# Kernel optimization log

Hardware: AMD Instinct MI355X
Metric: run time of the kernel (lower is better)

## Reference

```python
import jax, jax.numpy as jnp
import numpy as np

N_HEAD = 16
N_EMBD = 1024
TIME_EMBD = 64
EPS = 1e-5

def _ln(x, w, b):
    mu = jnp.mean(x, axis=-1, keepdims=True)
    var = jnp.mean(jnp.square(x - mu), axis=-1, keepdims=True)
    return (x - mu) * jax.lax.rsqrt(var + EPS) * w + b

def _gelu(x):
    return jax.nn.gelu(x, approximate=False)

def setup_inputs() -> dict:
    key = jax.random.key(0)
    ks = jax.random.split(key, 12)
    B, T, D, TE = 2, 2048, N_EMBD, TIME_EMBD
    C = D + TE  # 1088
    s = lambda fan_in: 1.0 / np.sqrt(fan_in)
    return {
        "z": jax.random.normal(ks[0], (B, T, D), jnp.float32),
        "t": jax.random.uniform(ks[1], (B,), jnp.float32),
        # time_mlp: Linear(1, TE) -> GELU -> Linear(TE, TE)
        "w_t1": jax.random.normal(ks[2], (1, TE), jnp.float32) * s(1),
        "b_t1": jnp.zeros((TE,), jnp.float32),
        "w_t2": jax.random.normal(ks[3], (TE, TE), jnp.float32) * s(TE),
        "b_t2": jnp.zeros((TE,), jnp.float32),
        # attention
        "ln_a_w": jnp.ones((C,), jnp.float32),
        "ln_a_b": jnp.zeros((C,), jnp.float32),
        "w_attn": jax.random.normal(ks[4], (C, 3 * D), jnp.float32) * s(C),
        "b_attn": jnp.zeros((3 * D,), jnp.float32),
        "w_proj": jax.random.normal(ks[5], (D, D), jnp.float32) * s(D),
        "b_proj": jnp.zeros((D,), jnp.float32),
        # mlp
        "ln_m_w": jnp.ones((C,), jnp.float32),
        "ln_m_b": jnp.zeros((C,), jnp.float32),
        "w_fc": jax.random.normal(ks[6], (C, 4 * D), jnp.float32) * s(C),
        "b_fc": jnp.zeros((4 * D,), jnp.float32),
        "w_fc2": jax.random.normal(ks[7], (4 * D, D), jnp.float32) * s(4 * D),
        "b_fc2": jnp.zeros((D,), jnp.float32),
    }

def reference(z, t, w_t1, b_t1, w_t2, b_t2, ln_a_w, ln_a_b, w_attn, b_attn,
              w_proj, b_proj, ln_m_w, ln_m_b, w_fc, b_fc, w_fc2, b_fc2):
    B, T, D = z.shape
    H, hd = N_HEAD, N_EMBD // N_HEAD
    # time embedding: [B, TE] broadcast over T
    t_emb = _gelu(t[:, None] @ w_t1 + b_t1) @ w_t2 + b_t2
    t_emb_bt = jnp.broadcast_to(t_emb[:, None, :], (B, T, TIME_EMBD))
    # --- attention with time-conditioned input ---
    zt = jnp.concatenate([z, t_emb_bt], axis=-1)            # [B,T,D+TE]
    x = _ln(zt, ln_a_w, ln_a_b)
    qkv = x @ w_attn + b_attn                               # [B,T,3D]
    q, k, v = jnp.split(qkv, 3, axis=-1)
    q = q.reshape(B, T, H, hd)
    k = k.reshape(B, T, H, hd)
    v = v.reshape(B, T, H, hd)
    att = jnp.einsum('bqhd,bkhd->bhqk', q, k) * (1.0 / np.sqrt(hd))
    mask = jnp.tril(jnp.ones((T, T), bool))
    att = jnp.where(mask, att, -jnp.inf)
    att = jax.nn.softmax(att, axis=-1)
    y = jnp.einsum('bhqk,bkhd->bqhd', att, v).reshape(B, T, D)
    h = y @ w_proj + b_proj                                 # [B,T,D]
    # --- mlp with time-conditioned input ---
    ht = jnp.concatenate([h, t_emb_bt], axis=-1)
    m = _ln(ht, ln_m_w, ln_m_b)
    dz = _gelu(m @ w_fc + b_fc) @ w_fc2 + b_fc2             # [B,T,D]
    return dz
```

## Files before the change

kernel.cpp:

```cpp
#include <hip/hip_runtime.h>
#include <stdint.h>
#include <math.h>

#define T_SEQ 2048
#define NHEAD 16
#define HD 64
#define DMODEL 1024
#define CDIM 1088
#define MROWS 4096

typedef uint16_t u16;
typedef __bf16 b8v __attribute__((ext_vector_type(8)));
typedef float f4v __attribute__((ext_vector_type(4)));

typedef __attribute__((address_space(3))) void lds_void;
typedef const __attribute__((address_space(1))) void glb_void;

#define GLL(g, l) __builtin_amdgcn_global_load_lds((glb_void*)(g), (lds_void*)(l), 16, 0, 0)

__device__ __forceinline__ float b2f(u16 u) {
  union { uint32_t i; float f; } c; c.i = ((uint32_t)u) << 16; return c.f;
}
__device__ __forceinline__ u16 f2b(float f) {
  union { float f; uint32_t i; } c; c.f = f;
  uint32_t x = c.i;
  return (u16)((x + 0x7fffu + ((x >> 16) & 1u)) >> 16);
}
__device__ __forceinline__ uint32_t cvt_pk_bf16(float lo, float hi) {
  uint32_t r;
  asm("v_cvt_pk_bf16_f32 %0, %1, %2" : "=v"(r) : "v"(lo), "v"(hi));
  return r;
}
__device__ __forceinline__ float exp2_hw(float x) {
  return __builtin_amdgcn_exp2f(x);
}
__device__ __forceinline__ float gelu_f(float x) {
  float ax = fabsf(x);
  float xs = ax * 0.70710678118654752f;
  float t = __frcp_rn(1.0f + 0.3275911f * xs);
  float poly = ((((1.061405429f * t - 1.453152027f) * t + 1.421413741f) * t
                 - 0.284496736f) * t + 0.254829592f) * t;
  float e = __expf(-xs * xs);
  float er = 1.0f - poly * e;
  er = copysignf(er, x);
  return 0.5f * x * (1.0f + er);
}

__global__ void time_mlp_kernel(const float* __restrict__ t, const float* __restrict__ w1,
                                const float* __restrict__ b1, const float* __restrict__ w2,
                                const float* __restrict__ b2, float* __restrict__ temb) {
  __shared__ float h1[2][64];
  int tid = threadIdx.x;
  int b = tid >> 6, i = tid & 63;
  float tv = t[b];
  h1[b][i] = gelu_f(tv * w1[i] + b1[i]);
  __syncthreads();
  float acc = b2[i];
  for (int k = 0; k < 64; ++k) acc += h1[b][k] * w2[k * 64 + i];
  temb[b * 64 + i] = acc;
}

__global__ __launch_bounds__(256) void transpose_kernel(const float* __restrict__ src,
                                                        u16* __restrict__ dst,
                                                        int R, int C) {
  __shared__ u16 tile[32][33];
  int tx = threadIdx.x & 31, ty = threadIdx.x >> 5;
  int c0 = blockIdx.x * 32, r0 = blockIdx.y * 32;
#pragma unroll
  for (int i = 0; i < 4; ++i) {
    int r = ty + i * 8;
    tile[r][tx] = f2b(src[(size_t)(r0 + r) * C + c0 + tx]);
  }
  __syncthreads();
#pragma unroll
  for (int i = 0; i < 4; ++i) {
    int c = ty + i * 8;
    dst[(size_t)(c0 + c) * R + r0 + tx] = tile[tx][c];
  }
}

__global__ __launch_bounds__(256) void add4_kernel(const float4* __restrict__ a,
                                                   const float4* __restrict__ b,
                                                   const float4* __restrict__ c,
                                                   const float4* __restrict__ d,
                                                   float4* __restrict__ o, int n4) {
  int i = blockIdx.x * 256 + threadIdx.x;
  if (i < n4) {
    float4 x = a[i], y = b[i], z = c[i], w = d[i];
    o[i] = float4{x.x + y.x + z.x + w.x, x.y + y.y + z.y + w.y,
                  x.z + y.z + z.z + w.z, x.w + y.w + z.w + w.w};
  }
}

__global__ __launch_bounds__(256) void ln_concat_kernel(const float* __restrict__ zf,
                                                        const float* __restrict__ zf2,
                                                        const float* __restrict__ temb,
                                                        const float* __restrict__ w,
                                                        const float* __restrict__ bvec,
                                                        u16* __restrict__ xout,
                                                        int mode) {
  __shared__ float red[4];
  int row = blockIdx.x;
  int b = row / T_SEQ;
  int tid = threadIdx.x;
  float v[5];
  float sum = 0.f;
#pragma unroll
  for (int i = 0; i < 5; ++i) {
    int c = tid + i * 256;
    float val = 0.f;
    if (c < CDIM) {
      if (c < DMODEL) {
        size_t idx = (size_t)row * DMODEL + c;
        if (mode == 1) val = zf[idx];
        else val = zf[idx] + zf2[idx];
      } else {
        val = temb[b * 64 + (c - DMODEL)];
      }
    }
    v[i] = val;
    sum += val;
  }
#pragma unroll
  for (int off = 32; off; off >>= 1) sum += __shfl_xor(sum, off, 64);
  int wv = tid >> 6, ln = tid & 63;
  if (ln == 0) red[wv] = sum;
  __syncthreads();
  float mean = (red[0] + red[1] + red[2] + red[3]) * (1.0f / CDIM);
  __syncthreads();
  float sq = 0.f;
#pragma unroll
  for (int i = 0; i < 5; ++i) {
    int c = tid + i * 256;
    if (c < CDIM) { float d = v[i] - mean; sq += d * d; }
  }
#pragma unroll
  for (int off = 32; off; off >>= 1) sq += __shfl_xor(sq, off, 64);
  if (ln == 0) red[wv] = sq;
  __syncthreads();
  float inv = rsqrtf((red[0] + red[1] + red[2] + red[3]) * (1.0f / CDIM) + 1e-5f);
#pragma unroll
  for (int i = 0; i < 5; ++i) {
    int c = tid + i * 256;
    if (c < CDIM)
      xout[(size_t)row * CDIM + c] = f2b((v[i] - mean) * inv * w[c] + bvec[c]);
  }
}

__global__ __launch_bounds__(512, 2) void gemm256_kernel(
    const u16* __restrict__ A, const u16* __restrict__ Bt,
    const float* __restrict__ bias,
    void* __restrict__ c0, void* __restrict__ c1,
    void* __restrict__ c2, void* __restrict__ c3,
    int M, int N, int K, int k_tiles, int do_gelu, int out_f32) {
  __shared__ u16 As[2][256 * 64];
  __shared__ u16 Bs[2][256 * 64];
  const int tid = threadIdx.x;
  const int wave = tid >> 6, lane = tid & 63;
  const int wr = wave >> 2, wc = wave & 3;
  const int lrow = lane & 15, quad = lane >> 4;

  int nxy = gridDim.x * gridDim.y;
  int bid = blockIdx.y * gridDim.x + blockIdx.x;
  int cpx = nxy >> 3;
  int swz = (bid & 7) * cpx + (bid >> 3);
  int bx = swz % gridDim.x, by = swz / gridDim.x;
  const int m0 = bx * 256, n0 = by * 256;
  const int kz = blockIdx.z;
  const int kb = kz * k_tiles * 64;
  const int NT = k_tiles;

  const int sr = tid >> 3;
  const int sc = ((tid & 7) ^ ((tid >> 3) & 7)) * 8;
  const u16* gA = A + (size_t)(m0 + sr) * K + kb + sc;
  const u16* gB = Bt + (size_t)(n0 + sr) * K + kb + sc;

  f4v acc[8][4] = {};
  b8v bq[2][4];

  auto STAGE_A = [&](int t, int h) {
    const u16* g = gA + (size_t)(h * 128) * K + t * 64;
    u16* l = (u16*)As[t & 1] + h * 8192 + (wave << 9);
    GLL(g, l);
    GLL(g + (size_t)64 * K, l + 4096);
  };
  auto STAGE_B = [&](int t, int h) {
    const u16* g = gB + (size_t)(h * 128) * K + t * 64;
    u16* l = (u16*)Bs[t & 1] + h * 8192 + (wave << 9);
    GLL(g, l);
    GLL(g + (size_t)64 * K, l + 4096);
  };

  STAGE_A(0, 0); STAGE_B(0, 0); STAGE_B(0, 1);
  STAGE_A(0, 1);
  if (NT > 1) { STAGE_A(1, 0); STAGE_B(1, 0); STAGE_B(1, 1); }
  if (NT > 1) asm volatile("s_waitcnt vmcnt(8)" ::: "memory");
  else        asm volatile("s_waitcnt vmcnt(2)" ::: "memory");
  __builtin_amdgcn_s_barrier();

  for (int t = 0; t < NT; ++t) {
    const char* abase = (const char*)As[t & 1];
    const char* bbase = (const char*)Bs[t & 1];
    const int asw = (lrow & 7) << 4;
    b8v af[4];

#pragma unroll
    for (int j = 0; j < 4; ++j)
      af[j] = *(const b8v*)(abase + (j * 32 + wr * 16 + lrow) * 128 + ((quad * 16) ^ asw));
#pragma unroll
    for (int n = 0; n < 4; ++n)
      bq[0][n] = *(const b8v*)(bbase + (wc * 64 + n * 16 + lrow) * 128 + ((quad * 16) ^ asw));
    if (t + 1 < NT) STAGE_A(t + 1, 1);
    __builtin_amdgcn_s_barrier();
    __builtin_amdgcn_s_setprio(1);
#pragma unroll
    for (int j = 0; j < 4; ++j)
#pragma unroll
      for (int n = 0; n < 4; ++n)
        acc[j][n] = __builtin_amdgcn_mfma_f32_16x16x32_bf16(bq[0][n], af[j], acc[j][n], 0, 0, 0);
    __builtin_amdgcn_s_setprio(0);
    __builtin_amdgcn_s_barrier();

#pragma unroll
    for (int j = 0; j < 4; ++j)
      af[j] = *(const b8v*)(abase + (j * 32 + wr * 16 + lrow) * 128 + ((64 + quad * 16) ^ asw));
#pragma unroll
    for (int n = 0; n < 4; ++n)
      bq[1][n] = *(const b8v*)(bbase + (wc * 64 + n * 16 + lrow) * 128 + ((64 + quad * 16) ^ asw));
    __builtin_amdgcn_s_barrier();
    __builtin_amdgcn_s_setprio(1);
#pragma unroll
    for (int j = 0; j < 4; ++j)
#pragma unroll
      for (int n = 0; n < 4; ++n)
        acc[j][n] = __builtin_amdgcn_mfma_f32_16x16x32_bf16(bq[1][n], af[j], acc[j][n], 0, 0, 0);
    __builtin_amdgcn_s_setprio(0);
    if (t + 1 < NT) asm volatile("s_waitcnt vmcnt(8)" ::: "memory");
    else            asm volatile("s_waitcnt vmcnt(0)" ::: "memory");
    __builtin_amdgcn_s_barrier();

#pragma unroll
    for (int j = 0; j < 4; ++j)
      af[j] = *(const b8v*)(abase + (128 + j * 32 + wr * 16 + lrow) * 128 + ((quad * 16) ^ asw));
    if (t + 2 < NT) { STAGE_B(t + 2, 0); STAGE_A(t + 2, 0); }
    __builtin_amdgcn_s_barrier();
    __builtin_amdgcn_s_setprio(1);
#pragma unroll
    for (int j = 0; j < 4; ++j)
#pragma unroll
      for (int n = 0; n < 4; ++n)
        acc[4 + j][n] = __builtin_amdgcn_mfma_f32_16x16x32_bf16(bq[0][n], af[j], acc[4 + j][n], 0, 0, 0);
    __builtin_amdgcn_s_setprio(0);
    __builtin_amdgcn_s_barrier();

#pragma unroll
    for (int j = 0; j < 4; ++j)
      af[j] = *(const b8v*)(abase + (128 + j * 32 + wr * 16 + lrow) * 128 + ((64 + quad * 16) ^ asw));
    if (t + 2 < NT) STAGE_B(t + 2, 1);
    __builtin_amdgcn_s_barrier();
    __builtin_amdgcn_s_setprio(1);
#pragma unroll
    for (int j = 0; j < 4; ++j)
#pragma unroll
      for (int n = 0; n < 4; ++n)
        acc[4 + j][n] = __builtin_amdgcn_mfma_f32_16x16x32_bf16(bq[1][n], af[j], acc[4 + j][n], 0, 0, 0);
    __builtin_amdgcn_s_setprio(0);
    if (t + 1 < NT) {
      if (t + 2 < NT) asm volatile("s_waitcnt vmcnt(8)" ::: "memory");
      else            asm volatile("s_waitcnt vmcnt(2)" ::: "memory");
    }
    __builtin_amdgcn_s_barrier();
  }

  void* Cout = (kz == 0) ? c0 : (kz == 1) ? c1 : (kz == 2) ? c2 : c3;
#pragma unroll
  for (int mh = 0; mh < 2; ++mh)
#pragma unroll
    for (int j = 0; j < 4; ++j) {
      int grow = m0 + mh * 128 + j * 32 + wr * 16 + lrow;
      size_t rb = (size_t)grow * N;
#pragma unroll
      for (int n = 0; n < 4; ++n) {
        int gcol = n0 + wc * 64 + n * 16 + quad * 4;
        float b0 = 0.f, b1 = 0.f, b2 = 0.f, b3 = 0.f;
        if (kz == 0) {
          float4 bv = *(const float4*)(bias + gcol);
          b0 = bv.x; b1 = bv.y; b2 = bv.z; b3 = bv.w;
        }
        f4v a = acc[mh * 4 + j][n];
        float v0 = a[0] + b0, v1 = a[1] + b1, v2 = a[2] + b2, v3 = a[3] + b3;
        if (do_gelu) {
          v0 = gelu_f(v0); v1 = gelu_f(v1); v2 = gelu_f(v2); v3 = gelu_f(v3);
        }
        if (out_f32) {
          *(float4*)((float*)Cout + rb + gcol) = float4{v0, v1, v2, v3};
        } else {
          ushort4 ov;
          ov.x = f2b(v0); ov.y = f2b(v1); ov.z = f2b(v2); ov.w = f2b(v3);
          *(ushort4*)((u16*)Cout + rb + gcol) = ov;
        }
      }
    }
}

__global__ __launch_bounds__(256) void gemm_splitk2_kernel(const u16* __restrict__ A,
                                                           const u16* __restrict__ Bt,
                                                           const float* __restrict__ bias,
                                                           float* __restrict__ C0,
                                                           float* __restrict__ C1,
                                                           int M, int N, int K, int Kc) {
  __shared__ u16 As[2][128 * 32];
  __shared__ u16 Bs[2][128 * 32];
  const int tid = threadIdx.x;
  const int wave = tid >> 6, lane = tid & 63;
  const int wr = wave >> 1, wc = wave & 1;
  const int m0 = blockIdx.x * 128;
  const int n0 = blockIdx.y * 128;
  const int kz = blockIdx.z;
  const int lrow = lane & 15, quad = lane >> 4;
  const int srow = lane >> 2, sseg = lane & 3;

  const u16* gA0 = A  + (size_t)(m0 + wave * 32 + srow) * K + kz * Kc + sseg * 8;
  const u16* gA1 = gA0 + (size_t)16 * K;
  const u16* gB0 = Bt + (size_t)(n0 + wave * 32 + srow) * K + kz * Kc + sseg * 8;
  const u16* gB1 = gB0 + (size_t)16 * K;
  const int la0 = (wave * 32) * 32, la1 = (wave * 32 + 16) * 32;

  f4v acc[4][4] = {};

  GLL(gA0, &As[0][la0]); GLL(gA1, &As[0][la1]);
  GLL(gB0, &Bs[0][la0]); GLL(gB1, &Bs[0][la1]);

  int cur = 0;
  for (int k0 = 0; k0 < Kc; k0 += 32) {
    __syncthreads();
    if (k0 + 32 < Kc) {
      int nxt = cur ^ 1;
      GLL(gA0 + k0 + 32, &As[nxt][la0]); GLL(gA1 + k0 + 32, &As[nxt][la1]);
      GLL(gB0 + k0 + 32, &Bs[nxt][la0]); GLL(gB1 + k0 + 32, &Bs[nxt][la1]);
    }
    b8v af[4], bfr[4];
#pragma unroll
    for (int mi = 0; mi < 4; ++mi)
      af[mi] = *(const b8v*)(&As[cur][(wr * 64 + mi * 16 + lrow) * 32 + quad * 8]);
#pragma unroll
    for (int ni = 0; ni < 4; ++ni)
      bfr[ni] = *(const b8v*)(&Bs[cur][(wc * 64 + ni * 16 + lrow) * 32 + quad * 8]);
#pragma unroll
    for (int mi = 0; mi < 4; ++mi)
#pragma unroll
      for (int ni = 0; ni < 4; ++ni)
        acc[mi][ni] = __builtin_amdgcn_mfma_f32_16x16x32_bf16(bfr[ni], af[mi], acc[mi][ni], 0, 0, 0);
    cur ^= 1;
  }

  float* C = kz ? C1 : C0;
#pragma unroll
  for (int mi = 0; mi < 4; ++mi) {
    int grow = m0 + wr * 64 + mi * 16 + lrow;
    size_t rb = (size_t)grow * N;
#pragma unroll
    for (int ni = 0; ni < 4; ++ni) {
      int gcol = n0 + wc * 64 + ni * 16 + quad * 4;
      float b0 = 0.f, b1 = 0.f, b2 = 0.f, b3 = 0.f;
      if (kz == 0) {
        float4 bv = *(const float4*)(bias + gcol);
        b0 = bv.x; b1 = bv.y; b2 = bv.z; b3 = bv.w;
      }
      *(float4*)(C + rb + gcol) = float4{acc[mi][ni][0] + b0, acc[mi][ni][1] + b1,
                                         acc[mi][ni][2] + b2, acc[mi][ni][3] + b3};
    }
  }
}

__global__ __launch_bounds__(512) void attn_mfma_kernel(const u16* __restrict__ qkv,
                                                        u16* __restrict__ y) {
  __shared__ u16 Ks[64 * 72];
  __shared__ u16 Vts[64 * 72];
  __shared__ u16 Ps[128 * 72];
  const int bh = blockIdx.x;
  const int b = bh >> 4, h = bh & 15;
  const int qt = 15 - (int)blockIdx.y;
  const int tid = threadIdx.x, w = tid >> 6, lane = tid & 63;
  const int lrow = lane & 15, quad = lane >> 4;
  const int q0 = qt * 128;
  const int qg = q0 + w * 16 + lrow;
  const int dchunk = 2 * qt + (w >> 2);

  b8v qf[2];
#pragma unroll
  for (int dc = 0; dc < 2; ++dc)
    qf[dc] = *(const b8v*)(qkv + (size_t)(b * T_SEQ + qg) * 3072 + h * 64 + dc * 32 + quad * 8);

  f4v oacc[4] = {};
  float mrun = -__builtin_inff(), lrun = 0.f;
  const float SC = 0.18033688011112042f;

  const int nch = 2 * qt + 2;
  for (int ct = 0; ct < nch; ++ct) {
    __syncthreads();
    {
      int r = tid >> 3, sg = tid & 7;
      const u16* src = qkv + (size_t)(b * T_SEQ + ct * 64 + r) * 3072 + h * 64 + 1024 + sg * 8;
      *(uint4*)(&Ks[r * 72 + sg * 8]) = *(const uint4*)(src);
    }
    {
      int pr = tid >> 4, half = (tid >> 3) & 1, dsg = tid & 7;
      int d0 = dsg * 8 + half * 4;
      const u16* v0 = qkv + (size_t)(b * T_SEQ + ct * 64 + 2 * pr) * 3072 + h * 64 + 2048 + d0;
      uint2 a = *(const uint2*)(v0);
      uint2 bb = *(const uint2*)(v0 + 3072);
      int keyp = (2 * pr) ^ (dsg * 8);
      u16* vb = &Vts[d0 * 72 + keyp];
      *(uint32_t*)(vb)           = __builtin_amdgcn_perm(bb.x, a.x, 0x05040100u);
      *(uint32_t*)(vb + 72)      = __builtin_amdgcn_perm(bb.x, a.x, 0x07060302u);
      *(uint32_t*)(vb + 144)     = __builtin_amdgcn_perm(bb.y, a.y, 0x05040100u);
      *(uint32_t*)(vb + 216)     = __builtin_amdgcn_perm(bb.y, a.y, 0x07060302u);
    }
    __syncthreads();
    if (ct > dchunk) continue;

    f4v sacc[4] = {};
#pragma unroll
    for (int ks = 0; ks < 4; ++ks)
#pragma unroll
      for (int dc = 0; dc < 2; ++dc) {
        b8v kf = *(const b8v*)(&Ks[(ks * 16 + lrow) * 72 + dc * 32 + quad * 8]);
        sacc[ks] = __builtin_amdgcn_mfma_f32_16x16x32_bf16(kf, qf[dc], sacc[ks], 0, 0, 0);
      }

    if (ct == dchunk) {
#pragma unroll
      for (int ks = 0; ks < 4; ++ks)
#pragma unroll
        for (int r = 0; r < 4; ++r) {
          int key = ct * 64 + ks * 16 + quad * 4 + r;
          if (key > qg) sacc[ks][r] = -__builtin_inff();
        }
    }

    float rmax = sacc[0][0];
#pragma unroll
    for (int ks = 0; ks < 4; ++ks)
#pragma unroll
      for (int r = 0; r < 4; ++r) rmax = fmaxf(rmax, sacc[ks][r]);
    rmax = fmaxf(rmax, __shfl_xor(rmax, 16, 64));
    rmax = fmaxf(rmax, __shfl_xor(rmax, 32, 64));
    rmax *= SC;
    float mn = fmaxf(mrun, rmax);
    float al = exp2_hw(mrun - mn);
    mrun = mn;
    float psum = 0.f;
#pragma unroll
    for (int ks = 0; ks < 4; ++ks) {
      float p0 = exp2_hw(fmaf(sacc[ks][0], SC, -mn));
      float p1 = exp2_hw(fmaf(sacc[ks][1], SC, -mn));
      float p2 = exp2_hw(fmaf(sacc[ks][2], SC, -mn));
      float p3 = exp2_hw(fmaf(sacc[ks][3], SC, -mn));
      psum += (p0 + p1) + (p2 + p3);
      uint2 pw;
      pw.x = cvt_pk_bf16(p0, p1);
      pw.y = cvt_pk_bf16(p2, p3);
      *(uint2*)(&Ps[(w * 16 + lrow) * 72 + ks * 16 + quad * 4]) = pw;
    }
    psum += __shfl_xor(psum, 16, 64);
    psum += __shfl_xor(psum, 32, 64);
    lrun = lrun * al + psum;
#pragma unroll
    for (int ds = 0; ds < 4; ++ds) oacc[ds] *= al;

    b8v pf[2];
#pragma unroll
    for (int kc = 0; kc < 2; ++kc)
      pf[kc] = *(const b8v*)(&Ps[(w * 16 + lrow) * 72 + kc * 32 + quad * 8]);
#pragma unroll
    for (int ds = 0; ds < 4; ++ds)
#pragma unroll
      for (int kc = 0; kc < 2; ++kc) {
        int d = ds * 16 + lrow;
        int off = (kc * 32 + quad * 8) ^ (((d >> 3) & 7) * 8);
        b8v vfv = *(const b8v*)(&Vts[d * 72 + off]);
        oacc[ds] = __builtin_amdgcn_mfma_f32_16x16x32_bf16(vfv, pf[kc], oacc[ds], 0, 0, 0);
      }
  }

  float rinv = 1.0f / lrun;
  u16* yrow = y + (size_t)(b * T_SEQ + qg) * DMODEL + h * 64;
#pragma unroll
  for (int ds = 0; ds < 4; ++ds) {
    uint2 ov;
    ov.x = cvt_pk_bf16(oacc[ds][0] * rinv, oacc[ds][1] * rinv);
    ov.y = cvt_pk_bf16(oacc[ds][2] * rinv, oacc[ds][3] * rinv);
    *(uint2*)(yrow + ds * 16 + quad * 4) = ov;
  }
}

extern "C" void kernel_launch(void* const* d_in, const int* in_sizes, int n_in,
                              void* d_out, int out_size, void* d_ws, size_t ws_size,
                              hipStream_t stream) {
  const float* z      = (const float*)d_in[0];
  const float* t      = (const float*)d_in[1];
  const float* w_t1   = (const float*)d_in[2];
  const float* b_t1   = (const float*)d_in[3];
  const float* w_t2   = (const float*)d_in[4];
  const float* b_t2   = (const float*)d_in[5];
  const float* ln_a_w = (const float*)d_in[6];
  const float* ln_a_b = (const float*)d_in[7];
  const float* w_attn = (const float*)d_in[8];
  const float* b_attn = (const float*)d_in[9];
  const float* w_proj = (const float*)d_in[10];
  const float* b_proj = (const float*)d_in[11];
  const float* ln_m_w = (const float*)d_in[12];
  const float* ln_m_b = (const float*)d_in[13];
  const float* w_fc   = (const float*)d_in[14];
  const float* b_fc   = (const float*)d_in[15];
  const float* w_fc2  = (const float*)d_in[16];
  const float* b_fc2  = (const float*)d_in[17];

  char* ws = (char*)d_ws;
  float* temb  = (float*)ws;
  u16* wT_attn = (u16*)(ws + 1024);
  u16* wT_proj = wT_attn + (size_t)3072 * 1088;
  u16* wT_fc   = wT_proj + (size_t)1024 * 1024;
  u16* wT_fc2  = wT_fc   + (size_t)4096 * 1088;
  u16* xbuf    = wT_fc2  + (size_t)1024 * 4096;
  u16* big     = xbuf    + (size_t)4096 * 1088;
  u16* ybuf    = big     + (size_t)4096 * 4096;
  float* p0    = (float*)(ybuf + (size_t)4096 * 1024);
  float* p1    = p0 + (size_t)4096 * 1024;
  float* p3    = (float*)wT_attn;

  time_mlp_kernel<<<dim3(1), dim3(128), 0, stream>>>(t, w_t1, b_t1, w_t2, b_t2, temb);

  transpose_kernel<<<dim3(3072 / 32, 1088 / 32), dim3(256), 0, stream>>>(w_attn, wT_attn, 1088, 3072);
  transpose_kernel<<<dim3(1024 / 32, 1024 / 32), dim3(256), 0, stream>>>(w_proj, wT_proj, 1024, 1024);
  transpose_kernel<<<dim3(4096 / 32, 1088 / 32), dim3(256), 0, stream>>>(w_fc, wT_fc, 1088, 4096);
  transpose_kernel<<<dim3(1024 / 32, 4096 / 32), dim3(256), 0, stream>>>(w_fc2, wT_fc2, 4096, 1024);

  ln_concat_kernel<<<dim3(MROWS), dim3(256), 0, stream>>>(
      z, (const float*)nullptr, temb, ln_a_w, ln_a_b, xbuf, 1);

  gemm256_kernel<<<dim3(16, 12, 1), dim3(512), 0, stream>>>(
      xbuf, wT_attn, b_attn, big, nullptr, nullptr, nullptr,
      MROWS, 3072, 1088, 17, 0, 0);

  attn_mfma_kernel<<<dim3(32, 16), dim3(512), 0, stream>>>(big, ybuf);

  gemm_splitk2_kernel<<<dim3(MROWS / 128, 1024 / 128, 2), dim3(256), 0, stream>>>(
      ybuf, wT_proj, b_proj, p0, p1, MROWS, 1024, 1024, 512);

  ln_concat_kernel<<<dim3(MROWS), dim3(256), 0, stream>>>(
      p0, p1, temb, ln_m_w, ln_m_b, xbuf, 2);

  gemm256_kernel<<<dim3(16, 16, 1), dim3(512), 0, stream>>>(
      xbuf, wT_fc, b_fc, big, nullptr, nullptr, nullptr,
      MROWS, 4096, 1088, 17, 1, 0);

  gemm256_kernel<<<dim3(16, 4, 4), dim3(512), 0, stream>>>(
      big, wT_fc2, b_fc2, p0, p1, d_out, p3,
      MROWS, 1024, 4096, 16, 0, 1);

  add4_kernel<<<dim3(MROWS * 1024 / 4 / 256), dim3(256), 0, stream>>>(
      (const float4*)p0, (const float4*)p1, (const float4*)d_out, (const float4*)p3,
      (float4*)d_out, MROWS * 1024 / 4);
}
```

Measured before the change: 385.7 us.

## Double-buffer K/V tiles in attention with register prefetch and smaller query tiles

Restructures the causal attention kernel to use 64-query tiles with 256 threads and twice as many blocks, so no wave sits idle on the diagonal chunk. K/V tiles are prefetched into registers for the next chunk while the current one computes, then written into a second LDS buffer, leaving one barrier per iteration instead of two. s_setprio is raised around the MFMA sections. The aim is to hide global load latency and cut wasted waves, at the cost of more LDS and registers per block.

```diff
diff --git a/kernel.cpp b/kernel.cpp
--- a/kernel.cpp
+++ b/kernel.cpp
@@ -373,19 +373,48 @@
   }
 }
 
-__global__ __launch_bounds__(512) void attn_mfma_kernel(const u16* __restrict__ qkv,
+__global__ __launch_bounds__(256) void attn_mfma_kernel(const u16* __restrict__ qkv,
                                                         u16* __restrict__ y) {
-  __shared__ u16 Ks[64 * 72];
-  __shared__ u16 Vts[64 * 72];
-  __shared__ u16 Ps[128 * 72];
+  __shared__ u16 Ks[2][64 * 72];
+  __shared__ u16 Vts[2][64 * 72];
+  __shared__ u16 Ps[64 * 72];
   const int bh = blockIdx.x;
   const int b = bh >> 4, h = bh & 15;
-  const int qt = 15 - (int)blockIdx.y;
+  const int qt = 31 - (int)blockIdx.y;
   const int tid = threadIdx.x, w = tid >> 6, lane = tid & 63;
   const int lrow = lane & 15, quad = lane >> 4;
-  const int q0 = qt * 128;
+  const int q0 = qt * 64;
   const int qg = q0 + w * 16 + lrow;
-  const int dchunk = 2 * qt + (w >> 2);
+
+  const int kr = tid >> 2, ksg = tid & 3;
+  const int pr = tid >> 3, dsg = tid & 7;
+  const u16* kbase = qkv + (size_t)(b * T_SEQ + kr) * 3072 + h * 64 + 1024 + ksg * 16;
+  const u16* vbase = qkv + (size_t)(b * T_SEQ + 2 * pr) * 3072 + h * 64 + 2048 + dsg * 8;
+  const int keyp = (2 * pr) ^ (dsg * 8);
+  const int d0 = dsg * 8;
+
+  uint4 krg0, krg1, vrg0, vrg1;
+  auto LOADR = [&](int ct) {
+    const u16* ksrc = kbase + (size_t)ct * 64 * 3072;
+    krg0 = *(const uint4*)(ksrc);
+    krg1 = *(const uint4*)(ksrc + 8);
+    const u16* vsrc = vbase + (size_t)ct * 64 * 3072;
+    vrg0 = *(const uint4*)(vsrc);
+    vrg1 = *(const uint4*)(vsrc + 3072);
+  };
+  auto WRITE = [&](int bi) {
+    *(uint4*)(&Ks[bi][kr * 72 + ksg * 16]) = krg0;
+    *(uint4*)(&Ks[bi][kr * 72 + ksg * 16 + 8]) = krg1;
+    uint32_t aw[4] = {vrg0.x, vrg0.y, vrg0.z, vrg0.w};
+    uint32_t bw[4] = {vrg1.x, vrg1.y, vrg1.z, vrg1.w};
+#pragma unroll
+    for (int m = 0; m < 4; ++m) {
+      *(uint32_t*)(&Vts[bi][(d0 + 2 * m) * 72 + keyp]) =
+          __builtin_amdgcn_perm(bw[m], aw[m], 0x05040100u);
+      *(uint32_t*)(&Vts[bi][(d0 + 2 * m + 1) * 72 + keyp]) =
+          __builtin_amdgcn_perm(bw[m], aw[m], 0x07060302u);
+    }
+  };
 
   b8v qf[2];
 #pragma unroll
@@ -396,40 +425,27 @@
   float mrun = -__builtin_inff(), lrun = 0.f;
   const float SC = 0.18033688011112042f;
 
-  const int nch = 2 * qt + 2;
+  LOADR(0);
+  WRITE(0);
+  __syncthreads();
+
+  const int nch = qt + 1;
   for (int ct = 0; ct < nch; ++ct) {
-    __syncthreads();
-    {
-      int r = tid >> 3, sg = tid & 7;
-      const u16* src = qkv + (size_t)(b * T_SEQ + ct * 64 + r) * 3072 + h * 64 + 1024 + sg * 8;
-      *(uint4*)(&Ks[r * 72 + sg * 8]) = *(const uint4*)(src);
-    }
-    {
-      int pr = tid >> 4, half = (tid >> 3) & 1, dsg = tid & 7;
-      int d0 = dsg * 8 + half * 4;
-      const u16* v0 = qkv + (size_t)(b * T_SEQ + ct * 64 + 2 * pr) * 3072 + h * 64 + 2048 + d0;
-      uint2 a = *(const uint2*)(v0);
-      uint2 bb = *(const uint2*)(v0 + 3072);
-      int keyp = (2 * pr) ^ (dsg * 8);
-      u16* vb = &Vts[d0 * 72 + keyp];
-      *(uint32_t*)(vb)           = __builtin_amdgcn_perm(bb.x, a.x, 0x05040100u);
-      *(uint32_t*)(vb + 72)      = __builtin_amdgcn_perm(bb.x, a.x, 0x07060302u);
-      *(uint32_t*)(vb + 144)     = __builtin_amdgcn_perm(bb.y, a.y, 0x05040100u);
-      *(uint32_t*)(vb + 216)     = __builtin_amdgcn_perm(bb.y, a.y, 0x07060302u);
-    }
-    __syncthreads();
-    if (ct > dchunk) continue;
+    const int cur = ct & 1;
+    if (ct + 1 < nch) LOADR(ct + 1);
 
     f4v sacc[4] = {};
+    __builtin_amdgcn_s_setprio(1);
 #pragma unroll
     for (int ks = 0; ks < 4; ++ks)
 #pragma unroll
       for (int dc = 0; dc < 2; ++dc) {
-        b8v kf = *(const b8v*)(&Ks[(ks * 16 + lrow) * 72 + dc * 32 + quad * 8]);
+        b8v kf = *(const b8v*)(&Ks[cur][(ks * 16 + lrow) * 72 + dc * 32 + quad * 8]);
         sacc[ks] = __builtin_amdgcn_mfma_f32_16x16x32_bf16(kf, qf[dc], sacc[ks], 0, 0, 0);
       }
-
-    if (ct == dchunk) {
+    __builtin_amdgcn_s_setprio(0);
+
+    if (ct == qt) {
 #pragma unroll
       for (int ks = 0; ks < 4; ++ks)
 #pragma unroll
@@ -473,15 +489,22 @@
 #pragma unroll
     for (int kc = 0; kc < 2; ++kc)
       pf[kc] = *(const b8v*)(&Ps[(w * 16 + lrow) * 72 + kc * 32 + quad * 8]);
+    __builtin_amdgcn_s_setprio(1);
 #pragma unroll
     for (int ds = 0; ds < 4; ++ds)
 #pragma unroll
       for (int kc = 0; kc < 2; ++kc) {
         int d = ds * 16 + lrow;
         int off = (kc * 32 + quad * 8) ^ (((d >> 3) & 7) * 8);
-        b8v vfv = *(const b8v*)(&Vts[d * 72 + off]);
+        b8v vfv = *(const b8v*)(&Vts[cur][d * 72 + off]);
         oacc[ds] = __builtin_amdgcn_mfma_f32_16x16x32_bf16(vfv, pf[kc], oacc[ds], 0, 0, 0);
       }
+    __builtin_amdgcn_s_setprio(0);
+
+    if (ct + 1 < nch) {
+      WRITE((ct + 1) & 1);
+      __syncthreads();
+    }
   }
 
   float rinv = 1.0f / lrun;
@@ -544,7 +567,7 @@
       xbuf, wT_attn, b_attn, big, nullptr, nullptr, nullptr,
       MROWS, 3072, 1088, 17, 0, 0);
 
-  attn_mfma_kernel<<<dim3(32, 16), dim3(512), 0, stream>>>(big, ybuf);
+  attn_mfma_kernel<<<dim3(32, 32), dim3(256), 0, stream>>>(big, ybuf);
 
   gemm_splitk2_kernel<<<dim3(MROWS / 128, 1024 / 128, 2), dim3(256), 0, stream>>>(
       ybuf, wT_proj, b_proj, p0, p1, MROWS, 1024, 1024, 512);
```

New measurement: 376.3 us. 2.4% less time.
